# Optimization experiments

Measured on AMD Instinct MI355X. Metric: run time of the kernel, lower is better.

The kernel has to match this reference:

```python
import jax, jax.numpy as jnp
import numpy as np

BS = 131072
NX = 4       # num_dim_x (p, theta, v, omega)
NU = 1       # num_dim_control
H = 256      # n_hidden


def segway_dynamics(x):
    # x: [bs, 4] -> f: [bs, 4], g: [bs, 4, 1]
    theta, v, omega = x[:, 1], x[:, 2], x[:, 3]
    c, s = jnp.cos(theta), jnp.sin(theta)
    f2 = (c * (9.8 * s + 11.5 * v) + 68.4 * v - 1.2 * omega ** 2 * s) / (c - 24.7)
    f3 = (-58.8 * v * c - 243.5 * v - s * (208.3 + omega ** 2 * c)) / (c ** 2 - 24.7)
    f = jnp.stack([v, omega, f2, f3], axis=1)
    g2 = (-1.8 * c - 10.9) / (c - 24.7)
    g3 = (9.3 * c + 38.6) / (c ** 2 - 24.7)
    zero = jnp.zeros_like(g2)
    g = jnp.stack([zero, zero, g2, g3], axis=1)[:, :, None]
    return f, g


def setup_inputs() -> dict:
    key = jax.random.key(0)
    ks = jax.random.split(key, 13)
    d = {"x": jax.random.normal(ks[0], (BS, NX), dtype=jnp.float32)}
    shapes = {
        "Vw1": (H, NX), "Vb1": (H,),
        "Vw2": (H, H),  "Vb2": (H,),
        "Vw3": (H // 4, H), "Vb3": (H // 4,),
        "Uw1": (H, NX), "Ub1": (H,),
        "Uw2": (H, H),  "Ub2": (H,),
        "Uw3": (NU, H), "Ub3": (NU,),
    }
    for i, (name, shp) in enumerate(shapes.items()):
        d[name] = jax.random.normal(ks[i + 1], shp, dtype=jnp.float32) * 0.05
    return d


def reference(x, Vw1, Vb1, Vw2, Vb2, Vw3, Vb3, Uw1, Ub1, Uw2, Ub2, Uw3, Ub3):
    # --- Lyapunov value + analytic gradient ---
    a1 = jnp.tanh(x @ Vw1.T + Vb1)          # [bs, H]
    a2 = jnp.tanh(a1 @ Vw2.T + Vb2)         # [bs, H]
    a3 = jnp.tanh(a2 @ Vw3.T + Vb3)         # [bs, H//4]
    V = 0.5 * jnp.sum(a3 * a3, axis=1)      # [bs]
    # diag_embed(1-tanh^2) @ W  ==  (1-tanh^2)[:, :, None] * W  (no dense diag)
    D1 = (1.0 - a1 ** 2)[:, :, None] * Vw1[None]                          # [bs, H, 4]
    D2 = (1.0 - a2 ** 2)[:, :, None] * jnp.einsum('ij,bjk->bik', Vw2, D1)  # [bs, H, 4]
    D3 = (1.0 - a3 ** 2)[:, :, None] * jnp.einsum('ij,bjk->bik', Vw3, D2)  # [bs, H/4, 4]
    grad_V = jnp.einsum('bi,bij->bj', a3, D3)  # [bs, 4]

    # --- learned controls ---
    u1 = jnp.tanh(x @ Uw1.T + Ub1)
    u2 = jnp.tanh(u1 @ Uw2.T + Ub2)
    u = jnp.tanh(u2 @ Uw3.T + Ub3) * 20.0     # [bs, 1]

    # --- Lie derivatives / Vdot ---
    f, g = segway_dynamics(x)
    L_f_V = jnp.sum(grad_V * f, axis=1, keepdims=True)    # [bs, 1]
    L_g_V = jnp.einsum('bi,bic->bc', grad_V, g)           # [bs, 1]
    Vdot = (L_f_V + jnp.sum(L_g_V * u, axis=1, keepdims=True))[:, :, None]  # [bs,1,1]
    return u, V, Vdot
```

## Files before the change

kernel.cpp:

```cpp
#include <hip/hip_runtime.h>
#include <hip/hip_bf16.h>

#define BSZ 131072

typedef __bf16 v8bf __attribute__((ext_vector_type(8)));
typedef float f32x4 __attribute__((ext_vector_type(4)));

constexpr int RPB = 64;
constexpr int NTHREADS = 512;
constexpr int LDA = 264;

constexpr int OFF_B2T = 0;
constexpr int OFF_U2T = 65536;
constexpr int OFF_B2  = 131072;
constexpr int OFF_B3T = 196608;
constexpr int OFF_B3  = 212992;
constexpr int OFF_U3  = 229376;
constexpr int OFF_GV  = 233472;
constexpr int OFF_LV1 = 237568;
constexpr int OFF_LU1 = 245760;
constexpr int WS_ELEMS = 253952;

__device__ __forceinline__ float tanhf_fast(float x){
  float e = __expf(2.0f * x);
  return 1.0f - 2.0f / (e + 1.0f);
}

__device__ __forceinline__ __bf16 f2bf(float f){
  unsigned u = __builtin_bit_cast(unsigned, f);
  u += 0x8000u;
  unsigned short h = (unsigned short)(u >> 16);
  return __builtin_bit_cast(__bf16, h);
}

__global__ void prep_weights(const float* __restrict__ Vw2,
                             const float* __restrict__ Uw2,
                             const float* __restrict__ Vw3,
                             const float* __restrict__ Vw1,
                             const float* __restrict__ Uw1,
                             const float* __restrict__ Uw3,
                             __bf16* __restrict__ ws){
  int e = blockIdx.x * 256 + threadIdx.x;
  if (e >= WS_ELEMS) return;
  int idx, NT, base, mode; const float* W;
  if      (e <  65536){ idx = e;          W = Vw2; mode = 0; NT = 16; base = OFF_B2T; }
  else if (e < 131072){ idx = e - 65536;  W = Uw2; mode = 0; NT = 16; base = OFF_U2T; }
  else if (e < 196608){ idx = e - 131072; W = Vw2; mode = 1; NT = 16; base = OFF_B2;  }
  else if (e < 212992){ idx = e - 196608; W = Vw3; mode = 0; NT = 4;  base = OFF_B3T; }
  else if (e < 229376){ idx = e - 212992; W = Vw3; mode = 1; NT = 16; base = OFF_B3;  }
  else if (e < 233472){ idx = e - 229376; W = Uw3; mode = 2; NT = 1;  base = OFF_U3;  }
  else if (e < 237568){ idx = e - 233472; W = Vw1; mode = 3; NT = 1;  base = OFF_GV;  }
  else if (e < 245760){ idx = e - 237568; W = Vw1; mode = 4; NT = 16; base = OFF_LV1; }
  else                { idx = e - 245760; W = Uw1; mode = 4; NT = 16; base = OFF_LU1; }
  int j = idx & 7, l = (idx >> 3) & 63, f = idx >> 9;
  int nt = f % NT, ks = f / NT;
  int k = ks * 32 + (l >> 4) * 8 + j;
  int n = nt * 16 + (l & 15);
  float v;
  if      (mode == 0) v = W[n * 256 + k];
  else if (mode == 1) v = W[k * 256 + n];
  else if (mode == 2) v = (n == 0) ? W[k] : 0.0f;
  else if (mode == 3) v = (n < 4)  ? W[k * 4 + n] : 0.0f;
  else                v = (k < 4)  ? W[n * 4 + k] : 0.0f;
  ws[base + idx] = f2bf(v);
}

__global__ __launch_bounds__(NTHREADS, 4) void fused_clf(
    const float* __restrict__ x,
    const float* __restrict__ Vb1, const float* __restrict__ Vb2,
    const float* __restrict__ Vb3,
    const float* __restrict__ Ub1, const float* __restrict__ Ub2,
    const float* __restrict__ Ub3,
    const __bf16* __restrict__ ws,
    float* __restrict__ out)
{
  __shared__ __bf16 b1[RPB][LDA];
  __shared__ __bf16 b2[RPB][LDA];
  __shared__ union alignas(16) S3 {
    __bf16 b3[RPB][72];
    float  r4[8][RPB][4];
  } s3;
  __shared__ float  red[RPB][4];
  __shared__ float  utile[RPB];

  const int tid  = threadIdx.x;
  const int lane = tid & 63;
  const int wave = tid >> 6;
  const int quad = lane >> 4;
  const int l16  = lane & 15;
  const int row0 = blockIdx.x * RPB;

  v8bf xa[4];
  #pragma unroll
  for (int m = 0; m < 4; m++){
    v8bf z;
    #pragma unroll
    for (int j = 0; j < 8; j++) z[j] = (__bf16)0.0f;
    if (quad == 0){
      float4 xv = ((const float4*)x)[row0 + m*16 + l16];
      z[0] = f2bf(xv.x); z[1] = f2bf(xv.y); z[2] = f2bf(xv.z); z[3] = f2bf(xv.w);
    }
    xa[m] = z;
  }

  auto layer1m = [&](const __bf16* __restrict__ Bw, const float* __restrict__ bv,
                     __bf16 (*dst)[LDA]){
    const v8bf* B = (const v8bf*)Bw;
    v8bf bf0 = B[(wave*2 + 0)*64 + lane];
    v8bf bf1 = B[(wave*2 + 1)*64 + lane];
    f32x4 acc[4][2];
    #pragma unroll
    for (int m = 0; m < 4; m++){ f32x4 z={0.f,0.f,0.f,0.f}; acc[m][0]=z; acc[m][1]=z; }
    #pragma unroll
    for (int m = 0; m < 4; m++){
      acc[m][0] = __builtin_amdgcn_mfma_f32_16x16x32_bf16(xa[m], bf0, acc[m][0], 0,0,0);
      acc[m][1] = __builtin_amdgcn_mfma_f32_16x16x32_bf16(xa[m], bf1, acc[m][1], 0,0,0);
    }
    #pragma unroll
    for (int m = 0; m < 4; m++){
      int rb = m*16 + quad*4;
      #pragma unroll
      for (int nt = 0; nt < 2; nt++){
        int col = (wave*2 + nt)*16 + l16;
        float bvv = bv[col];
        #pragma unroll
        for (int r = 0; r < 4; r++)
          dst[rb + r][col] = f2bf(tanhf_fast(acc[m][nt][r] + bvv));
      }
    }
  };

  auto gemm256 = [&](const __bf16 (*A)[LDA], const __bf16* __restrict__ Bw,
                     const float* __restrict__ bias, __bf16 (*dst)[LDA], int epi){
    f32x4 acc[4][2];
    #pragma unroll
    for (int m = 0; m < 4; m++){ f32x4 z={0.f,0.f,0.f,0.f}; acc[m][0]=z; acc[m][1]=z; }
    const v8bf* B = (const v8bf*)Bw;
    #pragma unroll
    for (int kk = 0; kk < 8; kk++){
      v8bf a[4];
      #pragma unroll
      for (int m = 0; m < 4; m++)
        a[m] = *(const v8bf*)&A[m*16 + l16][kk*32 + quad*8];
      #pragma unroll
      for (int nt = 0; nt < 2; nt++){
        v8bf bf = B[(kk*16 + wave*2 + nt)*64 + lane];
        #pragma unroll
        for (int m = 0; m < 4; m++)
          acc[m][nt] = __builtin_amdgcn_mfma_f32_16x16x32_bf16(a[m], bf, acc[m][nt], 0,0,0);
      }
    }
    #pragma unroll
    for (int m = 0; m < 4; m++){
      int rb = m*16 + quad*4;
      #pragma unroll
      for (int nt = 0; nt < 2; nt++){
        int col = (wave*2 + nt)*16 + l16;
        float bvv = (epi == 0) ? bias[col] : 0.0f;
        #pragma unroll
        for (int r = 0; r < 4; r++){
          float v = acc[m][nt][r] + bvv;
          if (epi == 0){
            dst[rb + r][col] = f2bf(tanhf_fast(v));
          } else {
            float a1v = (float)dst[rb + r][col];
            dst[rb + r][col] = f2bf(v * (1.0f - a1v*a1v));
          }
        }
      }
    }
  };

  auto mfma_reduce = [&](const __bf16 (*A)[LDA], const __bf16* __restrict__ Bw,
                         int ncols){
    f32x4 acc[4];
    #pragma unroll
    for (int m = 0; m < 4; m++){ f32x4 z={0.f,0.f,0.f,0.f}; acc[m]=z; }
    const v8bf* B = (const v8bf*)Bw;
    v8bf bf = B[wave*64 + lane];
    #pragma unroll
    for (int m = 0; m < 4; m++){
      v8bf a = *(const v8bf*)&A[m*16 + l16][wave*32 + quad*8];
      acc[m] = __builtin_amdgcn_mfma_f32_16x16x32_bf16(a, bf, acc[m], 0,0,0);
    }
    if (l16 < ncols){
      #pragma unroll
      for (int m = 0; m < 4; m++)
        #pragma unroll
        for (int r = 0; r < 4; r++)
          s3.r4[wave][m*16 + quad*4 + r][l16] = acc[m][r];
    }
  };

  layer1m(ws + OFF_LU1, Ub1, b2);
  __syncthreads();
  gemm256(b2, ws + OFF_U2T, Ub2, b1, 0);
  __syncthreads();
  mfma_reduce(b1, ws + OFF_U3, 1);
  __syncthreads();
  if (tid < RPB){
    float z = Ub3[0];
    #pragma unroll
    for (int w = 0; w < 8; w++) z += s3.r4[w][tid][0];
    float u = tanhf_fast(z) * 20.0f;
    utile[tid] = u;
    out[row0 + tid] = u;
  }
  layer1m(ws + OFF_LV1, Vb1, b1);
  __syncthreads();
  gemm256(b1, ws + OFF_B2T, Vb2, b2, 0);
  __syncthreads();

  {
    const int mp = wave >> 2;
    const int nt = wave & 3;
    f32x4 acc[2];
    { f32x4 z={0.f,0.f,0.f,0.f}; acc[0]=z; acc[1]=z; }
    const v8bf* B = (const v8bf*)(ws + OFF_B3T);
    #pragma unroll
    for (int kk = 0; kk < 8; kk++){
      v8bf bf = B[(kk*4 + nt)*64 + lane];
      #pragma unroll
      for (int m2 = 0; m2 < 2; m2++){
        v8bf a = *(const v8bf*)&b2[(mp*2 + m2)*16 + l16][kk*32 + quad*8];
        acc[m2] = __builtin_amdgcn_mfma_f32_16x16x32_bf16(a, bf, acc[m2], 0,0,0);
      }
    }
    int col = nt*16 + l16;
    float bvv = Vb3[col];
    #pragma unroll
    for (int m2 = 0; m2 < 2; m2++){
      #pragma unroll
      for (int r = 0; r < 4; r++){
        int row = (mp*2 + m2)*16 + quad*4 + r;
        float t = tanhf_fast(acc[m2][r] + bvv);
        float sq = t * t;
        sq += __shfl_xor(sq, 1); sq += __shfl_xor(sq, 2);
        sq += __shfl_xor(sq, 4); sq += __shfl_xor(sq, 8);
        s3.b3[row][col] = f2bf(t * (1.0f - t*t));
        if (l16 == 0) red[row][nt] = sq;
      }
    }
  }
  __syncthreads();

  {
    f32x4 acc[4][2];
    #pragma unroll
    for (int m = 0; m < 4; m++){ f32x4 z={0.f,0.f,0.f,0.f}; acc[m][0]=z; acc[m][1]=z; }
    const v8bf* B = (const v8bf*)(ws + OFF_B3);
    #pragma unroll
    for (int kk = 0; kk < 2; kk++){
      v8bf a[4];
      #pragma unroll
      for (int m = 0; m < 4; m++)
        a[m] = *(const v8bf*)&s3.b3[m*16 + l16][kk*32 + quad*8];
      #pragma unroll
      for (int nt = 0; nt < 2; nt++){
        v8bf bf = B[(kk*16 + wave*2 + nt)*64 + lane];
        #pragma unroll
        for (int m = 0; m < 4; m++)
          acc[m][nt] = __builtin_amdgcn_mfma_f32_16x16x32_bf16(a[m], bf, acc[m][nt], 0,0,0);
      }
    }
    #pragma unroll
    for (int m = 0; m < 4; m++){
      int rb = m*16 + quad*4;
      #pragma unroll
      for (int nt = 0; nt < 2; nt++){
        int col = (wave*2 + nt)*16 + l16;
        #pragma unroll
        for (int r = 0; r < 4; r++){
          float a2v = (float)b2[rb + r][col];
          b2[rb + r][col] = f2bf(acc[m][nt][r] * (1.0f - a2v*a2v));
        }
      }
    }
    if (tid < RPB)
      out[BSZ + row0 + tid] = 0.5f * (red[tid][0] + red[tid][1] + red[tid][2] + red[tid][3]);
  }
  __syncthreads();

  gemm256(b2, ws + OFF_B2, nullptr, b1, 1);
  __syncthreads();
  mfma_reduce(b1, ws + OFF_GV, 4);
  __syncthreads();
  if (tid < 256){
    int b = tid >> 2, k2 = tid & 3;
    float s = 0.f;
    #pragma unroll
    for (int w = 0; w < 8; w++) s += s3.r4[w][b][k2];
    red[b][k2] = s;
  }
  __syncthreads();

  if (tid < RPB){
    float4 xv = ((const float4*)x)[row0 + tid];
    float th = xv.y, vv = xv.z, om = xv.w;
    float c = cosf(th), s = sinf(th);
    float dc  = c - 24.7f;
    float dc2 = c*c - 24.7f;
    float f2v = (c*(9.8f*s + 11.5f*vv) + 68.4f*vv - 1.2f*om*om*s) / dc;
    float f3v = (-58.8f*vv*c - 243.5f*vv - s*(208.3f + om*om*c)) / dc2;
    float g2v = (-1.8f*c - 10.9f) / dc;
    float g3v = (9.3f*c + 38.6f) / dc2;
    float Lf = red[tid][0]*vv + red[tid][1]*om + red[tid][2]*f2v + red[tid][3]*f3v;
    float Lg = red[tid][2]*g2v + red[tid][3]*g3v;
    out[2*BSZ + row0 + tid] = Lf + Lg * utile[tid];
  }
}

extern "C" void kernel_launch(void* const* d_in, const int* in_sizes, int n_in,
                              void* d_out, int out_size, void* d_ws, size_t ws_size,
                              hipStream_t stream) {
  const float* x   = (const float*)d_in[0];
  const float* Vw1 = (const float*)d_in[1];
  const float* Vb1 = (const float*)d_in[2];
  const float* Vw2 = (const float*)d_in[3];
  const float* Vb2 = (const float*)d_in[4];
  const float* Vw3 = (const float*)d_in[5];
  const float* Vb3 = (const float*)d_in[6];
  const float* Uw1 = (const float*)d_in[7];
  const float* Ub1 = (const float*)d_in[8];
  const float* Uw2 = (const float*)d_in[9];
  const float* Ub2 = (const float*)d_in[10];
  const float* Uw3 = (const float*)d_in[11];
  const float* Ub3 = (const float*)d_in[12];
  __bf16* ws = (__bf16*)d_ws;
  float* out = (float*)d_out;

  hipLaunchKernelGGL(prep_weights, dim3((WS_ELEMS + 255) / 256), dim3(256), 0, stream,
                     Vw2, Uw2, Vw3, Vw1, Uw1, Uw3, ws);
  hipLaunchKernelGGL(fused_clf, dim3(BSZ / RPB), dim3(NTHREADS), 0, stream,
                     x, Vb1, Vb2, Vb3, Ub1, Ub2, Ub3, ws, out);
}
```

Measured before the change: 201.3 us.

## Swap MFMA operands so epilogues store packed bf16 rows, use fast rcp

Swaps the A/B operands of every MFMA so each lane holds four consecutive feature columns of one row. Epilogues can then load bias as a vector and write two packed bf16 pairs with v_cvt_pk_bf16_f32 in one 8-byte LDS store, instead of four scalar 2-byte stores. The change also replaces divisions in tanh and the dynamics with hardware reciprocal, uses __sincosf, vectorizes red reads, and simplifies the V reduction shuffles. It trades some numerical accuracy in the fast reciprocal and sincos, and the wider LDS stores may change bank-conflict patterns.

```diff
diff --git a/kernel.cpp b/kernel.cpp
--- a/kernel.cpp
+++ b/kernel.cpp
@@ -23,7 +23,7 @@
 
 __device__ __forceinline__ float tanhf_fast(float x){
   float e = __expf(2.0f * x);
-  return 1.0f - 2.0f / (e + 1.0f);
+  return 1.0f - 2.0f * __builtin_amdgcn_rcpf(e + 1.0f);
 }
 
 __device__ __forceinline__ __bf16 f2bf(float f){
@@ -32,6 +32,14 @@
   unsigned short h = (unsigned short)(u >> 16);
   return __builtin_bit_cast(__bf16, h);
 }
+
+__device__ __forceinline__ unsigned pk2bf(float lo, float hi){
+  unsigned r;
+  asm("v_cvt_pk_bf16_f32 %0, %1, %2" : "=v"(r) : "v"(lo), "v"(hi));
+  return r;
+}
+__device__ __forceinline__ float bflo(unsigned u){ return __builtin_bit_cast(float, u << 16); }
+__device__ __forceinline__ float bfhi(unsigned u){ return __builtin_bit_cast(float, u & 0xffff0000u); }
 
 __global__ void prep_weights(const float* __restrict__ Vw2,
                              const float* __restrict__ Uw2,
@@ -74,14 +82,14 @@
     const __bf16* __restrict__ ws,
     float* __restrict__ out)
 {
-  __shared__ __bf16 b1[RPB][LDA];
-  __shared__ __bf16 b2[RPB][LDA];
+  __shared__ alignas(16) __bf16 b1[RPB][LDA];
+  __shared__ alignas(16) __bf16 b2[RPB][LDA];
   __shared__ union alignas(16) S3 {
     __bf16 b3[RPB][72];
     float  r4[8][RPB][4];
   } s3;
-  __shared__ float  red[RPB][4];
-  __shared__ float  utile[RPB];
+  __shared__ alignas(16) float red[RPB][4];
+  __shared__ float utile[RPB];
 
   const int tid  = threadIdx.x;
   const int lane = tid & 63;
@@ -103,6 +111,7 @@
     xa[m] = z;
   }
 
+
   auto layer1m = [&](const __bf16* __restrict__ Bw, const float* __restrict__ bv,
                      __bf16 (*dst)[LDA]){
     const v8bf* B = (const v8bf*)Bw;
@@ -113,19 +122,22 @@
     for (int m = 0; m < 4; m++){ f32x4 z={0.f,0.f,0.f,0.f}; acc[m][0]=z; acc[m][1]=z; }
     #pragma unroll
     for (int m = 0; m < 4; m++){
-      acc[m][0] = __builtin_amdgcn_mfma_f32_16x16x32_bf16(xa[m], bf0, acc[m][0], 0,0,0);
-      acc[m][1] = __builtin_amdgcn_mfma_f32_16x16x32_bf16(xa[m], bf1, acc[m][1], 0,0,0);
-    }
-    #pragma unroll
-    for (int m = 0; m < 4; m++){
-      int rb = m*16 + quad*4;
-      #pragma unroll
-      for (int nt = 0; nt < 2; nt++){
-        int col = (wave*2 + nt)*16 + l16;
-        float bvv = bv[col];
-        #pragma unroll
-        for (int r = 0; r < 4; r++)
-          dst[rb + r][col] = f2bf(tanhf_fast(acc[m][nt][r] + bvv));
+      acc[m][0] = __builtin_amdgcn_mfma_f32_16x16x32_bf16(bf0, xa[m], acc[m][0], 0,0,0);
+      acc[m][1] = __builtin_amdgcn_mfma_f32_16x16x32_bf16(bf1, xa[m], acc[m][1], 0,0,0);
+    }
+    #pragma unroll
+    for (int nt = 0; nt < 2; nt++){
+      const int f0 = (wave*2 + nt)*16 + quad*4;
+      f32x4 bvv = ((const f32x4*)bv)[f0 >> 2];
+      #pragma unroll
+      for (int m = 0; m < 4; m++){
+        const int brow = m*16 + l16;
+        uint2 pk;
+        pk.x = pk2bf(tanhf_fast(acc[m][nt][0] + bvv[0]),
+                     tanhf_fast(acc[m][nt][1] + bvv[1]));
+        pk.y = pk2bf(tanhf_fast(acc[m][nt][2] + bvv[2]),
+                     tanhf_fast(acc[m][nt][3] + bvv[3]));
+        *(uint2*)&dst[brow][f0] = pk;
       }
     }
   };
@@ -147,26 +159,33 @@
         v8bf bf = B[(kk*16 + wave*2 + nt)*64 + lane];
         #pragma unroll
         for (int m = 0; m < 4; m++)
-          acc[m][nt] = __builtin_amdgcn_mfma_f32_16x16x32_bf16(a[m], bf, acc[m][nt], 0,0,0);
-      }
-    }
-    #pragma unroll
-    for (int m = 0; m < 4; m++){
-      int rb = m*16 + quad*4;
-      #pragma unroll
-      for (int nt = 0; nt < 2; nt++){
-        int col = (wave*2 + nt)*16 + l16;
-        float bvv = (epi == 0) ? bias[col] : 0.0f;
-        #pragma unroll
-        for (int r = 0; r < 4; r++){
-          float v = acc[m][nt][r] + bvv;
-          if (epi == 0){
-            dst[rb + r][col] = f2bf(tanhf_fast(v));
-          } else {
-            float a1v = (float)dst[rb + r][col];
-            dst[rb + r][col] = f2bf(v * (1.0f - a1v*a1v));
-          }
+          acc[m][nt] = __builtin_amdgcn_mfma_f32_16x16x32_bf16(bf, a[m], acc[m][nt], 0,0,0);
+      }
+    }
+    #pragma unroll
+    for (int nt = 0; nt < 2; nt++){
+      const int f0 = (wave*2 + nt)*16 + quad*4;
+      f32x4 bvv = {0.f,0.f,0.f,0.f};
+      if (epi == 0) bvv = ((const f32x4*)bias)[f0 >> 2];
+      #pragma unroll
+      for (int m = 0; m < 4; m++){
+        const int brow = m*16 + l16;
+        uint2 pk;
+        if (epi == 0){
+          pk.x = pk2bf(tanhf_fast(acc[m][nt][0] + bvv[0]),
+                       tanhf_fast(acc[m][nt][1] + bvv[1]));
+          pk.y = pk2bf(tanhf_fast(acc[m][nt][2] + bvv[2]),
+                       tanhf_fast(acc[m][nt][3] + bvv[3]));
+        } else {
+          uint2 old = *(const uint2*)&dst[brow][f0];
+          float a0 = bflo(old.x), a1 = bfhi(old.x);
+          float c0 = bflo(old.y), c1 = bfhi(old.y);
+          pk.x = pk2bf(acc[m][nt][0] * (1.0f - a0*a0),
+                       acc[m][nt][1] * (1.0f - a1*a1));
+          pk.y = pk2bf(acc[m][nt][2] * (1.0f - c0*c0),
+                       acc[m][nt][3] * (1.0f - c1*c1));
         }
+        *(uint2*)&dst[brow][f0] = pk;
       }
     }
   };
@@ -181,14 +200,18 @@
     #pragma unroll
     for (int m = 0; m < 4; m++){
       v8bf a = *(const v8bf*)&A[m*16 + l16][wave*32 + quad*8];
-      acc[m] = __builtin_amdgcn_mfma_f32_16x16x32_bf16(a, bf, acc[m], 0,0,0);
-    }
-    if (l16 < ncols){
-      #pragma unroll
-      for (int m = 0; m < 4; m++)
+      acc[m] = __builtin_amdgcn_mfma_f32_16x16x32_bf16(bf, a, acc[m], 0,0,0);
+    }
+    if (quad == 0){
+      if (ncols == 4){
         #pragma unroll
-        for (int r = 0; r < 4; r++)
-          s3.r4[wave][m*16 + quad*4 + r][l16] = acc[m][r];
+        for (int m = 0; m < 4; m++)
+          *(f32x4*)&s3.r4[wave][m*16 + l16][0] = acc[m];
+      } else {
+        #pragma unroll
+        for (int m = 0; m < 4; m++)
+          s3.r4[wave][m*16 + l16][0] = acc[m][0];
+      }
     }
   };
 
@@ -223,23 +246,27 @@
       #pragma unroll
       for (int m2 = 0; m2 < 2; m2++){
         v8bf a = *(const v8bf*)&b2[(mp*2 + m2)*16 + l16][kk*32 + quad*8];
-        acc[m2] = __builtin_amdgcn_mfma_f32_16x16x32_bf16(a, bf, acc[m2], 0,0,0);
-      }
-    }
-    int col = nt*16 + l16;
-    float bvv = Vb3[col];
+        acc[m2] = __builtin_amdgcn_mfma_f32_16x16x32_bf16(bf, a, acc[m2], 0,0,0);
+      }
+    }
+    const int f0 = nt*16 + quad*4;
+    f32x4 bvv = ((const f32x4*)Vb3)[f0 >> 2];
     #pragma unroll
     for (int m2 = 0; m2 < 2; m2++){
-      #pragma unroll
-      for (int r = 0; r < 4; r++){
-        int row = (mp*2 + m2)*16 + quad*4 + r;
-        float t = tanhf_fast(acc[m2][r] + bvv);
-        float sq = t * t;
-        sq += __shfl_xor(sq, 1); sq += __shfl_xor(sq, 2);
-        sq += __shfl_xor(sq, 4); sq += __shfl_xor(sq, 8);
-        s3.b3[row][col] = f2bf(t * (1.0f - t*t));
-        if (l16 == 0) red[row][nt] = sq;
-      }
+      const int brow = (mp*2 + m2)*16 + l16;
+      float t0 = tanhf_fast(acc[m2][0] + bvv[0]);
+      float t1 = tanhf_fast(acc[m2][1] + bvv[1]);
+      float t2 = tanhf_fast(acc[m2][2] + bvv[2]);
+      float t3 = tanhf_fast(acc[m2][3] + bvv[3]);
+      float s0 = t0*t0, s1 = t1*t1, s2 = t2*t2, s3q = t3*t3;
+      float sq = (s0 + s1) + (s2 + s3q);
+      sq += __shfl_xor(sq, 16);
+      sq += __shfl_xor(sq, 32);
+      if (quad == 0) red[brow][nt] = sq;
+      uint2 pk;
+      pk.x = pk2bf(t0*(1.0f - s0), t1*(1.0f - s1));
+      pk.y = pk2bf(t2*(1.0f - s2), t3*(1.0f - s3q));
+      *(uint2*)&s3.b3[brow][f0] = pk;
     }
   }
   __syncthreads();
@@ -260,20 +287,24 @@
         v8bf bf = B[(kk*16 + wave*2 + nt)*64 + lane];
         #pragma unroll
         for (int m = 0; m < 4; m++)
-          acc[m][nt] = __builtin_amdgcn_mfma_f32_16x16x32_bf16(a[m], bf, acc[m][nt], 0,0,0);
-      }
-    }
-    #pragma unroll
-    for (int m = 0; m < 4; m++){
-      int rb = m*16 + quad*4;
-      #pragma unroll
-      for (int nt = 0; nt < 2; nt++){
-        int col = (wave*2 + nt)*16 + l16;
-        #pragma unroll
-        for (int r = 0; r < 4; r++){
-          float a2v = (float)b2[rb + r][col];
-          b2[rb + r][col] = f2bf(acc[m][nt][r] * (1.0f - a2v*a2v));
-        }
+          acc[m][nt] = __builtin_amdgcn_mfma_f32_16x16x32_bf16(bf, a[m], acc[m][nt], 0,0,0);
+      }
+    }
+    #pragma unroll
+    for (int nt = 0; nt < 2; nt++){
+      const int f0 = (wave*2 + nt)*16 + quad*4;
+      #pragma unroll
+      for (int m = 0; m < 4; m++){
+        const int brow = m*16 + l16;
+        uint2 old = *(const uint2*)&b2[brow][f0];
+        float a0 = bflo(old.x), a1 = bfhi(old.x);
+        float c0 = bflo(old.y), c1 = bfhi(old.y);
+        uint2 pk;
+        pk.x = pk2bf(acc[m][nt][0] * (1.0f - a0*a0),
+                     acc[m][nt][1] * (1.0f - a1*a1));
+        pk.y = pk2bf(acc[m][nt][2] * (1.0f - c0*c0),
+                     acc[m][nt][3] * (1.0f - c1*c1));
+        *(uint2*)&b2[brow][f0] = pk;
       }
     }
     if (tid < RPB)
@@ -297,15 +328,17 @@
   if (tid < RPB){
     float4 xv = ((const float4*)x)[row0 + tid];
     float th = xv.y, vv = xv.z, om = xv.w;
-    float c = cosf(th), s = sinf(th);
-    float dc  = c - 24.7f;
-    float dc2 = c*c - 24.7f;
-    float f2v = (c*(9.8f*s + 11.5f*vv) + 68.4f*vv - 1.2f*om*om*s) / dc;
-    float f3v = (-58.8f*vv*c - 243.5f*vv - s*(208.3f + om*om*c)) / dc2;
-    float g2v = (-1.8f*c - 10.9f) / dc;
-    float g3v = (9.3f*c + 38.6f) / dc2;
-    float Lf = red[tid][0]*vv + red[tid][1]*om + red[tid][2]*f2v + red[tid][3]*f3v;
-    float Lg = red[tid][2]*g2v + red[tid][3]*g3v;
+    float c, s;
+    __sincosf(th, &s, &c);
+    float rdc  = __builtin_amdgcn_rcpf(c - 24.7f);
+    float rdc2 = __builtin_amdgcn_rcpf(c*c - 24.7f);
+    float f2v = (c*(9.8f*s + 11.5f*vv) + 68.4f*vv - 1.2f*om*om*s) * rdc;
+    float f3v = (-58.8f*vv*c - 243.5f*vv - s*(208.3f + om*om*c)) * rdc2;
+    float g2v = (-1.8f*c - 10.9f) * rdc;
+    float g3v = (9.3f*c + 38.6f) * rdc2;
+    f32x4 rv = *(const f32x4*)&red[tid][0];
+    float Lf = rv[0]*vv + rv[1]*om + rv[2]*f2v + rv[3]*f3v;
+    float Lg = rv[2]*g2v + rv[3]*g3v;
     out[2*BSZ + row0 + tid] = Lf + Lg * utile[tid];
   }
 }
```

After: 166.3 us. 1.21x faster.
